# Optimization experiments

Measured on AMD Instinct MI355X. Metric: run time of the kernel, lower is better.

The kernel has to match this reference:

```python
import jax, jax.numpy as jnp
import numpy as np

B, H, S = 32, 128, 8192

def setup_inputs() -> dict:
    key = jax.random.key(0)
    k1, k2, k3, k4, k5 = jax.random.split(key, 5)
    return {
        "static_hidden": jax.random.normal(k1, (B, H, S), dtype=jnp.float32),
        "dynamic_hidden": jax.random.normal(k2, (B, H, S), dtype=jnp.float32),
        "decoder_hidden": jax.random.normal(k3, (B, H), dtype=jnp.float32),
        "v": jax.random.normal(k4, (1, 1, H), dtype=jnp.float32) * 0.01,
        "W": jax.random.normal(k5, (1, H, 3 * H), dtype=jnp.float32) * 0.01,
    }

def reference(static_hidden, dynamic_hidden, decoder_hidden, v, W):
    b, h, s = static_hidden.shape
    # concat (static, dynamic, expanded decoder) along feature dim -> [b, 3h, s]
    hidden = jnp.concatenate(
        [static_hidden, dynamic_hidden,
         jnp.broadcast_to(decoder_hidden[:, :, None], (b, h, s))], axis=1)
    # W[0]: [h, 3h]; tanh(W @ hidden) -> [b, h, s]
    e = jnp.tanh(jnp.einsum('hk,bks->bhs', W[0], hidden))
    # v[0,0]: [h]; scores -> [b, 1, s]
    scores = jnp.einsum('h,bhs->bs', v[0, 0], e)[:, None, :]
    return jax.nn.softmax(scores, axis=2)
```

## Files before the change

### kernel.cpp

```cpp
#include <hip/hip_runtime.h>
#include <math.h>

#define BB 32
#define HH 128
#define SS 8192

typedef __attribute__((ext_vector_type(8))) short bf8;
typedef __attribute__((ext_vector_type(4))) float f4;

static __device__ __forceinline__ unsigned short f2bf(float x) {
  union { float f; unsigned int u; } c; c.f = x;
  unsigned int r = c.u + 0x7FFFu + ((c.u >> 16) & 1u);
  return (unsigned short)(r >> 16);
}

__global__ __launch_bounds__(256) void prep_kernel(
    const float* __restrict__ W, const float* __restrict__ dec,
    unsigned short* __restrict__ Abf, float* __restrict__ bias) {
  const int b = blockIdx.x;
  const int tid = threadIdx.x;
  if (tid < HH) {
    const float* wr = W + (size_t)tid * 384 + 256;
    const float* db = dec + (size_t)b * HH;
    float acc = 0.f;
    #pragma unroll 8
    for (int j = 0; j < HH; ++j) acc += wr[j] * db[j];
    bias[b * HH + tid] = acc;
  }
  if (b == 0) {
    for (int idx = tid; idx < HH * 256; idx += 256) {
      int h = idx >> 8, k = idx & 255;
      Abf[idx] = f2bf(W[h * 384 + k]);
    }
  }
}

__global__ __launch_bounds__(64) void attn_main(
    const float* __restrict__ sta, const float* __restrict__ dyn,
    const unsigned short* __restrict__ Abf, const float* __restrict__ bias,
    const float* __restrict__ v, float* __restrict__ scores) {
  const int l    = threadIdx.x;
  const int b    = blockIdx.x >> 8;
  const int tile = blockIdx.x & 255;
  const int quad = l >> 4;
  const int n16  = l & 15;
  const int col0 = (tile << 5) + n16;

  const size_t base = ((size_t)b << 20) + ((size_t)(quad << 3)) * SS;
  const float* p0 = sta + base;
  const float* p1 = dyn + base;

  f4 acc[8][2];
  #pragma unroll
  for (int mt = 0; mt < 8; ++mt) {
    acc[mt][0] = (f4){0.f, 0.f, 0.f, 0.f};
    acc[mt][1] = (f4){0.f, 0.f, 0.f, 0.f};
  }

  float bcur[2][8], bnxt[2][8];

  auto loadB = [&](int step, float (&dst)[2][8]) {
    const float* tp = (step < 4 ? p0 : p1) + ((size_t)((step & 3) << 5)) * SS;
    #pragma unroll
    for (int nt = 0; nt < 2; ++nt) {
      const float* p = tp + col0 + (nt << 4);
      #pragma unroll
      for (int j = 0; j < 8; ++j)
        dst[nt][j] = p[(size_t)j * SS];
    }
  };

  loadB(0, bcur);
  #pragma unroll
  for (int step = 0; step < 8; ++step) {
    if (step < 7) loadB(step + 1, bnxt);
    bf8 bfr[2];
    #pragma unroll
    for (int nt = 0; nt < 2; ++nt) {
      bf8 t;
      #pragma unroll
      for (int j = 0; j < 8; ++j) t[j] = (short)f2bf(bcur[nt][j]);
      bfr[nt] = t;
    }
    const unsigned short* abase = Abf + ((size_t)n16 << 8) + (step << 5) + (quad << 3);
    #pragma unroll
    for (int mt = 0; mt < 8; ++mt) {
      bf8 af = *(const bf8*)(abase + (mt << 12));
      acc[mt][0] = __builtin_amdgcn_mfma_f32_16x16x32_bf16(af, bfr[0], acc[mt][0], 0, 0, 0);
      acc[mt][1] = __builtin_amdgcn_mfma_f32_16x16x32_bf16(af, bfr[1], acc[mt][1], 0, 0, 0);
    }
    if (step < 7) {
      #pragma unroll
      for (int nt = 0; nt < 2; ++nt)
        #pragma unroll
        for (int j = 0; j < 8; ++j) bcur[nt][j] = bnxt[nt][j];
    }
  }

  float part[2] = {0.f, 0.f};
  #pragma unroll
  for (int mt = 0; mt < 8; ++mt) {
    #pragma unroll
    for (int r = 0; r < 4; ++r) {
      const int h = mt * 16 + quad * 4 + r;
      const float bv = bias[(b << 7) + h];
      const float vv = v[h];
      #pragma unroll
      for (int nt = 0; nt < 2; ++nt) {
        float z = acc[mt][nt][r] + bv;
        part[nt] += vv * tanhf(z);
      }
    }
  }
  #pragma unroll
  for (int nt = 0; nt < 2; ++nt) {
    float p = part[nt];
    p += __shfl_xor(p, 16, 64);
    p += __shfl_xor(p, 32, 64);
    if (quad == 0)
      scores[((size_t)b << 13) + (tile << 5) + (nt << 4) + n16] = p;
  }
}

__global__ __launch_bounds__(1024) void softmax_kernel(float* __restrict__ out) {
  const int b = blockIdx.x;
  const int tid = threadIdx.x;
  float* row = out + ((size_t)b << 13);
  float4 x0 = ((const float4*)row)[tid];
  float4 x1 = ((const float4*)row)[tid + 1024];
  float lmax = fmaxf(fmaxf(fmaxf(x0.x, x0.y), fmaxf(x0.z, x0.w)),
                     fmaxf(fmaxf(x1.x, x1.y), fmaxf(x1.z, x1.w)));
  __shared__ float red[17];
  #pragma unroll
  for (int o = 32; o >= 1; o >>= 1) lmax = fmaxf(lmax, __shfl_xor(lmax, o, 64));
  if ((tid & 63) == 0) red[tid >> 6] = lmax;
  __syncthreads();
  if (tid < 64) {
    float m = (tid < 16) ? red[tid] : -3.0e38f;
    #pragma unroll
    for (int o = 8; o >= 1; o >>= 1) m = fmaxf(m, __shfl_xor(m, o, 64));
    if (tid == 0) red[16] = m;
  }
  __syncthreads();
  const float gmax = red[16];
  float e[8];
  e[0] = expf(x0.x - gmax); e[1] = expf(x0.y - gmax);
  e[2] = expf(x0.z - gmax); e[3] = expf(x0.w - gmax);
  e[4] = expf(x1.x - gmax); e[5] = expf(x1.y - gmax);
  e[6] = expf(x1.z - gmax); e[7] = expf(x1.w - gmax);
  float ls = e[0] + e[1] + e[2] + e[3] + e[4] + e[5] + e[6] + e[7];
  #pragma unroll
  for (int o = 32; o >= 1; o >>= 1) ls += __shfl_xor(ls, o, 64);
  __syncthreads();
  if ((tid & 63) == 0) red[tid >> 6] = ls;
  __syncthreads();
  if (tid < 64) {
    float m = (tid < 16) ? red[tid] : 0.f;
    #pragma unroll
    for (int o = 8; o >= 1; o >>= 1) m += __shfl_xor(m, o, 64);
    if (tid == 0) red[16] = m;
  }
  __syncthreads();
  const float inv = 1.0f / red[16];
  float4 o0 = make_float4(e[0] * inv, e[1] * inv, e[2] * inv, e[3] * inv);
  float4 o1 = make_float4(e[4] * inv, e[5] * inv, e[6] * inv, e[7] * inv);
  ((float4*)row)[tid] = o0;
  ((float4*)row)[tid + 1024] = o1;
}

extern "C" void kernel_launch(void* const* d_in, const int* in_sizes, int n_in,
                              void* d_out, int out_size, void* d_ws, size_t ws_size,
                              hipStream_t stream) {
  const float* sta = (const float*)d_in[0];
  const float* dyn = (const float*)d_in[1];
  const float* dec = (const float*)d_in[2];
  const float* v   = (const float*)d_in[3];
  const float* W   = (const float*)d_in[4];

  unsigned short* Abf = (unsigned short*)d_ws;
  float* bias = (float*)((char*)d_ws + 128 * 256 * 2);
  float* scores = (float*)d_out;

  prep_kernel<<<BB, 256, 0, stream>>>(W, dec, Abf, bias);
  attn_main<<<BB * (SS / 32), 64, 0, stream>>>(sta, dyn, Abf, bias, v, scores);
  softmax_kernel<<<BB, 1024, 0, stream>>>(scores);
}
```

Baseline: 386.6 us.

## Vectorize B loads as float2 with interleaved columns and pack four waves per block

Each lane now loads two adjacent columns with a float2 load instead of two scalar loads 16 columns apart. The MFMA column mapping becomes interleaved (even and odd columns), and the output is stored as float2 to match. Blocks now hold 4 waves of 256 threads instead of single-wave blocks, which cuts the block count and adds a launch_bounds occupancy hint. The goal is fewer memory instructions and better coalescing on the bandwidth-bound streaming read, at the risk of register-pressure changes from the occupancy hint.

```diff
diff --git a/kernel.cpp b/kernel.cpp
--- a/kernel.cpp
+++ b/kernel.cpp
@@ -35,18 +35,20 @@
   }
 }
 
-__global__ __launch_bounds__(64) void attn_main(
+__global__ __launch_bounds__(256, 4) void attn_main(
     const float* __restrict__ sta, const float* __restrict__ dyn,
     const unsigned short* __restrict__ Abf, const float* __restrict__ bias,
     const float* __restrict__ v, float* __restrict__ scores) {
-  const int l    = threadIdx.x;
-  const int b    = blockIdx.x >> 8;
-  const int tile = blockIdx.x & 255;
+  const int tid  = threadIdx.x;
+  const int l    = tid & 63;
+  const int gw   = (blockIdx.x << 2) + (tid >> 6);
+  const int b    = gw >> 8;
+  const int tile = gw & 255;
   const int quad = l >> 4;
   const int n16  = l & 15;
-  const int col0 = (tile << 5) + n16;
+  const int s0   = tile << 5;
 
-  const size_t base = ((size_t)b << 20) + ((size_t)(quad << 3)) * SS;
+  const size_t base = ((size_t)b << 20) + (size_t)(quad << 3) * SS + s0 + (n16 << 1);
   const float* p0 = sta + base;
   const float* p1 = dyn + base;
 
@@ -57,43 +59,35 @@
     acc[mt][1] = (f4){0.f, 0.f, 0.f, 0.f};
   }
 
-  float bcur[2][8], bnxt[2][8];
+  float2 bcur[8], bnxt[8];
 
-  auto loadB = [&](int step, float (&dst)[2][8]) {
+  auto loadB = [&](int step, float2 (&dst)[8]) {
     const float* tp = (step < 4 ? p0 : p1) + ((size_t)((step & 3) << 5)) * SS;
     #pragma unroll
-    for (int nt = 0; nt < 2; ++nt) {
-      const float* p = tp + col0 + (nt << 4);
-      #pragma unroll
-      for (int j = 0; j < 8; ++j)
-        dst[nt][j] = p[(size_t)j * SS];
-    }
+    for (int j = 0; j < 8; ++j)
+      dst[j] = *(const float2*)(tp + (size_t)j * SS);
   };
 
   loadB(0, bcur);
   #pragma unroll
   for (int step = 0; step < 8; ++step) {
     if (step < 7) loadB(step + 1, bnxt);
-    bf8 bfr[2];
+    bf8 bfr0, bfr1;
     #pragma unroll
-    for (int nt = 0; nt < 2; ++nt) {
-      bf8 t;
-      #pragma unroll
-      for (int j = 0; j < 8; ++j) t[j] = (short)f2bf(bcur[nt][j]);
-      bfr[nt] = t;
+    for (int j = 0; j < 8; ++j) {
+      bfr0[j] = (short)f2bf(bcur[j].x);
+      bfr1[j] = (short)f2bf(bcur[j].y);
     }
     const unsigned short* abase = Abf + ((size_t)n16 << 8) + (step << 5) + (quad << 3);
     #pragma unroll
     for (int mt = 0; mt < 8; ++mt) {
       bf8 af = *(const bf8*)(abase + (mt << 12));
-      acc[mt][0] = __builtin_amdgcn_mfma_f32_16x16x32_bf16(af, bfr[0], acc[mt][0], 0, 0, 0);
-      acc[mt][1] = __builtin_amdgcn_mfma_f32_16x16x32_bf16(af, bfr[1], acc[mt][1], 0, 0, 0);
+      acc[mt][0] = __builtin_amdgcn_mfma_f32_16x16x32_bf16(af, bfr0, acc[mt][0], 0, 0, 0);
+      acc[mt][1] = __builtin_amdgcn_mfma_f32_16x16x32_bf16(af, bfr1, acc[mt][1], 0, 0, 0);
     }
     if (step < 7) {
       #pragma unroll
-      for (int nt = 0; nt < 2; ++nt)
-        #pragma unroll
-        for (int j = 0; j < 8; ++j) bcur[nt][j] = bnxt[nt][j];
+      for (int j = 0; j < 8; ++j) bcur[j] = bnxt[j];
     }
   }
 
@@ -105,20 +99,17 @@
       const int h = mt * 16 + quad * 4 + r;
       const float bv = bias[(b << 7) + h];
       const float vv = v[h];
-      #pragma unroll
-      for (int nt = 0; nt < 2; ++nt) {
-        float z = acc[mt][nt][r] + bv;
-        part[nt] += vv * tanhf(z);
-      }
+      part[0] += vv * tanhf(acc[mt][0][r] + bv);
+      part[1] += vv * tanhf(acc[mt][1][r] + bv);
     }
   }
-  #pragma unroll
-  for (int nt = 0; nt < 2; ++nt) {
-    float p = part[nt];
-    p += __shfl_xor(p, 16, 64);
-    p += __shfl_xor(p, 32, 64);
-    if (quad == 0)
-      scores[((size_t)b << 13) + (tile << 5) + (nt << 4) + n16] = p;
+  part[0] += __shfl_xor(part[0], 16, 64);
+  part[0] += __shfl_xor(part[0], 32, 64);
+  part[1] += __shfl_xor(part[1], 16, 64);
+  part[1] += __shfl_xor(part[1], 32, 64);
+  if (quad == 0) {
+    float2 o = make_float2(part[0], part[1]);
+    *(float2*)(scores + ((size_t)b << 13) + s0 + (n16 << 1)) = o;
   }
 }
 
@@ -182,6 +173,6 @@
   float* scores = (float*)d_out;
 
   prep_kernel<<<BB, 256, 0, stream>>>(W, dec, Abf, bias);
-  attn_main<<<BB * (SS / 32), 64, 0, stream>>>(sta, dyn, Abf, bias, v, scores);
+  attn_main<<<BB * (SS / 32) / 4, 256, 0, stream>>>(sta, dyn, Abf, bias, v, scores);
   softmax_kernel<<<BB, 1024, 0, stream>>>(scores);
 }
```

Result: faster. 378.8 us (-2.0%).
